# Kernel tuning notes

Measured on AMD Instinct MI355X. Metric: run time of the kernel, lower is better.

Reference implementation:

```python
import jax, jax.numpy as jnp
import numpy as np

N = 14          # num_nodes (fixed by train_adj_14 / BatchNorm1d(14))
BN_EPS = 1e-5
COS_EPS = 1e-8  # torch.cosine_similarity norm clamp


def _leaky(y):
    return jnp.where(y >= 0, y, 0.2 * y)


def _gcn(x, adj, w, b):
    # DenseGCNConv with add_loop=True. adj: [N,N] or [B,N,N]; x: [B,N,F]
    eye = jnp.eye(N, dtype=adj.dtype)
    adj = adj * (1.0 - eye) + eye                    # set diagonal to 1
    d = jnp.clip(adj.sum(-1), 1.0, None) ** -0.5     # [.., N]
    adj = d[..., :, None] * adj * d[..., None, :]    # sym-normalized
    return jnp.matmul(adj, jnp.matmul(x, w)) + b


def _bn(y, gamma, beta):
    # BatchNorm1d(num_features=N) on [B, N, C], training-mode batch stats
    mu = y.mean(axis=(0, 2), keepdims=True)
    var = ((y - mu) ** 2).mean(axis=(0, 2), keepdims=True)
    yhat = (y - mu) * jax.lax.rsqrt(var + BN_EPS)
    return yhat * gamma[None, :, None] + beta[None, :, None]


def _corr(h):
    # vectorized abs cosine-similarity matrix, diag forced to 1
    sq = jnp.sum(h * h, axis=-1, keepdims=True)
    hn = h * jax.lax.rsqrt(jnp.maximum(sq, COS_EPS * COS_EPS))
    c = jnp.abs(jnp.einsum('bif,bjf->bij', hn, hn))
    eye = jnp.eye(N, dtype=c.dtype)
    return c * (1.0 - eye) + eye


def setup_inputs() -> dict:
    key = jax.random.key(0)
    ks = jax.random.split(key, 8)
    B, F_IN, F_OUT = 4096, 1024, 1024
    H = F_OUT // 2

    def sym(k):
        a = jax.random.uniform(k, (N, N), jnp.float32)
        return (a + a.T) * 0.5

    s_fc = (2.0 / (F_IN + F_OUT)) ** 0.5
    s1 = (6.0 / (F_IN + H)) ** 0.5
    s2 = (6.0 / (H + F_OUT)) ** 0.5
    return {
        'x': jax.random.normal(ks[0], (B, N, F_IN), jnp.float32),
        'adj1': sym(ks[1]),
        'adj2': sym(ks[2]),
        'fc_w': jax.random.normal(ks[3], (F_IN, F_OUT), jnp.float32) * s_fc,
        'fc_b': jnp.zeros((F_OUT,), jnp.float32),
        'gcn1_w': jax.random.uniform(ks[4], (F_IN, H), jnp.float32, -s1, s1),
        'gcn1_b': jnp.zeros((H,), jnp.float32),
        'gcn2_w': jax.random.uniform(ks[5], (H, F_OUT), jnp.float32, -s2, s2),
        'gcn2_b': jnp.zeros((F_OUT,), jnp.float32),
        'gamma1': jnp.ones((N,), jnp.float32), 'beta1': jnp.zeros((N,), jnp.float32),
        'gamma2': jnp.ones((N,), jnp.float32), 'beta2': jnp.zeros((N,), jnp.float32),
        'gamma3': jnp.ones((N,), jnp.float32), 'beta3': jnp.zeros((N,), jnp.float32),
    }


def reference(x, adj1, adj2, fc_w, fc_b, gcn1_w, gcn1_b, gcn2_w, gcn2_b,
              gamma1, beta1, gamma2, beta2, gamma3, beta3):
    h = _leaky(jnp.matmul(x, fc_w) + fc_b)           # fc + LeakyReLU(0.2)
    corr = _corr(h)                                   # [B,N,N]

    out = _leaky(_bn(_gcn(x, adj1, gcn1_w, gcn1_b), gamma1, beta1))
    out3 = _leaky(_bn(_gcn(x, adj2, gcn1_w, gcn1_b), gamma3, beta3))
    out4 = _leaky(_bn(_gcn(out3, corr, gcn2_w, gcn2_b), gamma2, beta2))
    out2 = _leaky(_bn(_gcn(out, corr, gcn2_w, gcn2_b), gamma2, beta2))

    return (out2 + out4, corr, h)
```

## Files before the change

### kernel.cpp

```cpp
#include <hip/hip_runtime.h>
#include <stdint.h>

typedef __attribute__((ext_vector_type(8))) short short8;
typedef __attribute__((ext_vector_type(4))) float floatx4;

#define B_SZ 4096
#define M1 57344
#define M2 114688
#define NCAT 1536

#define OFF_XB    ((size_t)0)
#define OFF_BCAT  ((size_t)117440512)
#define OFF_W2T   ((size_t)120586240)
#define OFF_T     ((size_t)121634816)
#define OFF_ADJN  ((size_t)356515840)
#define OFF_ADJC  ((size_t)356517888)
#define OFF_PART1 ((size_t)359729152)
#define OFF_PART2 ((size_t)360646656)
#define OFF_SS1   ((size_t)361564160)
#define OFF_SS2   ((size_t)361564416)

__device__ __forceinline__ unsigned short f2bf(float f){
  union { float f; uint32_t u; } v; v.f = f;
  uint32_t r = (v.u + 0x7FFFu + ((v.u >> 16) & 1u)) >> 16;
  return (unsigned short)r;
}
__device__ __forceinline__ float bf2f(unsigned short s){
  union { uint32_t u; float f; } v; v.u = ((uint32_t)s) << 16; return v.f;
}
__device__ __forceinline__ float leaky(float y){ return y >= 0.0f ? y : 0.2f*y; }
__device__ __forceinline__ void gl2lds16(const void* g, void* l){
  __builtin_amdgcn_global_load_lds(
      (const __attribute__((address_space(1))) unsigned int*)g,
      (__attribute__((address_space(3))) unsigned int*)l, 16, 0, 0);
}

__global__ void k_prep_adj(const float* __restrict__ adj1, const float* __restrict__ adj2,
                           float* __restrict__ adjn){
  __shared__ float a[392];
  __shared__ float d[28];
  int tid = threadIdx.x;
  for (int e = tid; e < 392; e += 256){
    int t = e / 196, ij = e % 196, i = ij / 14, j = ij % 14;
    const float* src = t ? adj2 : adj1;
    a[e] = (i == j) ? 1.0f : src[ij];
  }
  __syncthreads();
  if (tid < 28){
    int t = tid / 14, i = tid % 14;
    float s = 0.f;
    for (int j = 0; j < 14; j++) s += a[t*196 + i*14 + j];
    d[tid] = rsqrtf(fmaxf(s, 1.0f));
  }
  __syncthreads();
  for (int e = tid; e < 392; e += 256){
    int t = e / 196, ij = e % 196, i = ij / 14, j = ij % 14;
    adjn[e] = d[t*14+i] * a[e] * d[t*14+j];
  }
}

__global__ void k_convert_x(const float4* __restrict__ x4, uint2* __restrict__ xb4, int n4){
  int stride = gridDim.x * blockDim.x;
  for (int i = blockIdx.x*blockDim.x + threadIdx.x; i < n4; i += stride){
    float4 f = x4[i];
    uint2 o;
    o.x = (uint32_t)f2bf(f.x) | ((uint32_t)f2bf(f.y) << 16);
    o.y = (uint32_t)f2bf(f.z) | ((uint32_t)f2bf(f.w) << 16);
    xb4[i] = o;
  }
}

__global__ void k_convert_w(const float* __restrict__ fcw, const float* __restrict__ w1,
                            const float* __restrict__ w2, unsigned short* __restrict__ bcatT,
                            unsigned short* __restrict__ w2T){
  int idx = blockIdx.x*blockDim.x + threadIdx.x;
  if (idx < NCAT*1024){
    int n = idx >> 10, k = idx & 1023;
    float v = (n < 1024) ? fcw[k*1024 + n] : w1[k*512 + (n - 1024)];
    bcatT[idx] = f2bf(v);
  } else {
    int r = idx - NCAT*1024;
    int n = r >> 9, k = r & 511;
    w2T[r] = f2bf(w2[k*1024 + n]);
  }
}

template<int MODE>
__global__ __launch_bounds__(256)
void k_gemm_bt(const unsigned short* __restrict__ A, const unsigned short* __restrict__ Bt,
               int K, const float* __restrict__ bias,
               float* __restrict__ h_out, unsigned short* __restrict__ o_bf16){
  __shared__ unsigned short As[4096];
  __shared__ unsigned short Bs[4096];
  int tid = threadIdx.x;
  int lane = tid & 63, wave = tid >> 6;
  int wm = wave & 1, wn = wave >> 1;
  int bm = blockIdx.x, bn = blockIdx.y;
  const unsigned short* aptr = A  + (size_t)(bm*128 + (tid >> 2))*K + (tid & 3)*8;
  const unsigned short* bptr = Bt + (size_t)(bn*128 + (tid >> 2))*K + (tid & 3)*8;
  unsigned short* asd = &As[tid*8];
  unsigned short* bsd = &Bs[tid*8];
  size_t row64 = (size_t)64 * K;
  int fr = lane & 15, fq = lane >> 4;
  floatx4 acc[4][4] = {};
  for (int k0 = 0; k0 < K; k0 += 32){
    __syncthreads();
    gl2lds16(aptr + k0,         asd);
    gl2lds16(aptr + k0 + row64, asd + 2048);
    gl2lds16(bptr + k0,         bsd);
    gl2lds16(bptr + k0 + row64, bsd + 2048);
    __syncthreads();
    short8 af[4], bq[4];
    #pragma unroll
    for (int i = 0; i < 4; i++)
      af[i] = *(const short8*)&As[(wm*64 + i*16 + fr)*32 + fq*8];
    #pragma unroll
    for (int j = 0; j < 4; j++)
      bq[j] = *(const short8*)&Bs[(wn*64 + j*16 + fr)*32 + fq*8];
    #pragma unroll
    for (int i = 0; i < 4; i++)
      #pragma unroll
      for (int j = 0; j < 4; j++)
        acc[i][j] = __builtin_amdgcn_mfma_f32_16x16x32_bf16(af[i], bq[j], acc[i][j], 0, 0, 0);
  }
  #pragma unroll
  for (int i = 0; i < 4; i++){
    #pragma unroll
    for (int j = 0; j < 4; j++){
      int n  = bn*128 + wn*64 + j*16 + fr;
      int mb = bm*128 + wm*64 + i*16 + fq*4;
      #pragma unroll
      for (int r = 0; r < 4; r++){
        int m = mb + r;
        float c = acc[i][j][r];
        if (MODE == 1){
          if (n < 1024){
            c += bias[n];
            h_out[(size_t)m*1024 + n] = leaky(c);
          } else {
            o_bf16[(size_t)m*512 + (n - 1024)] = f2bf(c);
          }
        } else {
          o_bf16[(size_t)m*1024 + n] = f2bf(c);
        }
      }
    }
  }
}

__global__ __launch_bounds__(256)
void k_corr(const float* __restrict__ h, float* __restrict__ corr, float* __restrict__ adjc){
  __shared__ float G[4][16][17];
  __shared__ float C[4][14][15];
  __shared__ float dd[4][16];
  int lane = threadIdx.x & 63, wave = threadIdx.x >> 6;
  int b = blockIdx.x*4 + wave;
  int r = lane & 15, q = lane >> 4;
  const float* hrow = h + (size_t)(b*14 + r)*1024 + q*8;
  bool valid = r < 14;
  floatx4 acc = {0.f, 0.f, 0.f, 0.f};
  for (int k0 = 0; k0 < 1024; k0 += 32){
    short8 f = {0,0,0,0,0,0,0,0};
    if (valid){
      float4 f0 = *(const float4*)(hrow + k0);
      float4 f1 = *(const float4*)(hrow + k0 + 4);
      f[0] = (short)f2bf(f0.x); f[1] = (short)f2bf(f0.y);
      f[2] = (short)f2bf(f0.z); f[3] = (short)f2bf(f0.w);
      f[4] = (short)f2bf(f1.x); f[5] = (short)f2bf(f1.y);
      f[6] = (short)f2bf(f1.z); f[7] = (short)f2bf(f1.w);
    }
    acc = __builtin_amdgcn_mfma_f32_16x16x32_bf16(f, f, acc, 0, 0, 0);
  }
  #pragma unroll
  for (int t = 0; t < 4; t++) G[wave][q*4 + t][r] = acc[t];
  __syncthreads();
  if (lane < 14) dd[wave][lane] = rsqrtf(fmaxf(G[wave][lane][lane], 1e-16f));
  __syncthreads();
  for (int e = lane; e < 196; e += 64){
    int i = e / 14, j = e % 14;
    float c = (i == j) ? 1.0f : fabsf(G[wave][i][j]) * dd[wave][i] * dd[wave][j];
    C[wave][i][j] = c;
    corr[(size_t)b*196 + e] = c;
  }
  __syncthreads();
  if (lane < 14){
    float s = 0.f;
    #pragma unroll
    for (int j = 0; j < 14; j++) s += C[wave][lane][j];
    dd[wave][lane] = rsqrtf(fmaxf(s, 1.0f));
  }
  __syncthreads();
  for (int e = lane; e < 196; e += 64){
    int i = e / 14, j = e % 14;
    adjc[(size_t)b*196 + e] = C[wave][i][j] * dd[wave][i] * dd[wave][j];
  }
}

__global__ __launch_bounds__(256)
void k_stats1(const unsigned short* __restrict__ t1, const float* __restrict__ adjn,
              const float* __restrict__ b1, float* __restrict__ part){
  __shared__ float adjs[392];
  __shared__ float red[56*4];
  int tid = threadIdx.x, b = blockIdx.x;
  for (int e = tid; e < 392; e += 256) adjs[e] = adjn[e];
  __syncthreads();
  int cc = tid*2;
  const unsigned short* base = t1 + (size_t)b*14*512 + cc;
  float v0[14], v1[14];
  #pragma unroll
  for (int m = 0; m < 14; m++){
    unsigned int u = *(const unsigned int*)(base + m*512);
    v0[m] = bf2f((unsigned short)(u & 0xffffu));
    v1[m] = bf2f((unsigned short)(u >> 16));
  }
  float bias0 = b1[cc], bias1 = b1[cc+1];
  float vals[56];
  #pragma unroll
  for (int br = 0; br < 2; br++){
    #pragma unroll
    for (int n = 0; n < 14; n++){
      float p0 = bias0, p1 = bias1;
      const float* arow = &adjs[br*196 + n*14];
      #pragma unroll
      for (int m = 0; m < 14; m++){ p0 += arow[m]*v0[m]; p1 += arow[m]*v1[m]; }
      vals[(br*14 + n)*2 + 0] = p0 + p1;
      vals[(br*14 + n)*2 + 1] = p0*p0 + p1*p1;
    }
  }
  int lane = tid & 63, wave = tid >> 6;
  #pragma unroll
  for (int i = 0; i < 56; i++){
    float x = vals[i];
    #pragma unroll
    for (int off = 32; off > 0; off >>= 1) x += __shfl_down(x, off, 64);
    if (lane == 0) red[i*4 + wave] = x;
  }
  __syncthreads();
  if (tid < 56)
    part[(size_t)tid*4096 + b] = red[tid*4] + red[tid*4+1] + red[tid*4+2] + red[tid*4+3];
}

__global__ void k_finalize(const float* __restrict__ part, const float* __restrict__ gA,
                           const float* __restrict__ bA, const float* __restrict__ gB,
                           const float* __restrict__ bB, float inv_count,
                           float* __restrict__ ss){
  int j = blockIdx.x, tid = threadIdx.x;
  const float* ps = part + (size_t)(j*2)*4096;
  const float* pq = ps + 4096;
  float s = 0.f, q = 0.f;
  for (int e = tid; e < 4096; e += 256){ s += ps[e]; q += pq[e]; }
  __shared__ float rs[4], rq[4];
  int lane = tid & 63, wave = tid >> 6;
  #pragma unroll
  for (int off = 32; off > 0; off >>= 1){ s += __shfl_down(s,off,64); q += __shfl_down(q,off,64); }
  if (lane == 0){ rs[wave] = s; rq[wave] = q; }
  __syncthreads();
  if (tid == 0){
    s = rs[0]+rs[1]+rs[2]+rs[3];
    q = rq[0]+rq[1]+rq[2]+rq[3];
    float mu = s * inv_count;
    float var = q * inv_count - mu*mu;
    float rsig = rsqrtf(var + 1e-5f);
    int br = j / 14, n = j % 14;
    float g  = br ? gB[n] : gA[n];
    float be = br ? bB[n] : bA[n];
    float scale = rsig * g;
    ss[j*2]   = scale;
    ss[j*2+1] = be - mu*scale;
  }
}

__global__ __launch_bounds__(256)
void k_apply1(const unsigned short* __restrict__ t1, const float* __restrict__ adjn,
              const float* __restrict__ b1, const float* __restrict__ ss,
              unsigned short* __restrict__ outcat){
  __shared__ float adjs[392];
  __shared__ float sss[56];
  int tid = threadIdx.x, b = blockIdx.x;
  for (int e = tid; e < 392; e += 256) adjs[e] = adjn[e];
  if (tid < 56) sss[tid] = ss[tid];
  __syncthreads();
  int cc = tid*2;
  const unsigned short* base = t1 + (size_t)b*14*512 + cc;
  float v0[14], v1[14];
  #pragma unroll
  for (int m = 0; m < 14; m++){
    unsigned int u = *(const unsigned int*)(base + m*512);
    v0[m] = bf2f((unsigned short)(u & 0xffffu));
    v1[m] = bf2f((unsigned short)(u >> 16));
  }
  float bias0 = b1[cc], bias1 = b1[cc+1];
  #pragma unroll
  for (int br = 0; br < 2; br++){
    #pragma unroll
    for (int n = 0; n < 14; n++){
      float p0 = bias0, p1 = bias1;
      const float* arow = &adjs[br*196 + n*14];
      #pragma unroll
      for (int m = 0; m < 14; m++){ p0 += arow[m]*v0[m]; p1 += arow[m]*v1[m]; }
      float scale = sss[(br*14+n)*2], shift = sss[(br*14+n)*2+1];
      float y0 = leaky(p0*scale + shift);
      float y1 = leaky(p1*scale + shift);
      size_t row = (size_t)br*M1 + (size_t)b*14 + n;
      *(unsigned int*)(outcat + row*512 + cc) =
          (uint32_t)f2bf(y0) | ((uint32_t)f2bf(y1) << 16);
    }
  }
}

__global__ __launch_bounds__(512)
void k_stats2(const unsigned short* __restrict__ t2, const float* __restrict__ adjc,
              const float* __restrict__ b2, float* __restrict__ part){
  __shared__ float adjs[196];
  __shared__ float red[28*8];
  int tid = threadIdx.x, b = blockIdx.x;
  for (int e = tid; e < 196; e += 512) adjs[e] = adjc[(size_t)b*196 + e];
  __syncthreads();
  int cc = tid*2;
  float bias0 = b2[cc], bias1 = b2[cc+1];
  int lane = tid & 63, wave = tid >> 6;
  for (int half = 0; half < 2; half++){
    const unsigned short* base = t2 + ((size_t)half*M1 + (size_t)b*14)*1024 + cc;
    float v0[14], v1[14];
    #pragma unroll
    for (int m = 0; m < 14; m++){
      unsigned int u = *(const unsigned int*)(base + (size_t)m*1024);
      v0[m] = bf2f((unsigned short)(u & 0xffffu));
      v1[m] = bf2f((unsigned short)(u >> 16));
    }
    float vals[28];
    #pragma unroll
    for (int n = 0; n < 14; n++){
      float p0 = bias0, p1 = bias1;
      const float* arow = &adjs[n*14];
      #pragma unroll
      for (int m = 0; m < 14; m++){ p0 += arow[m]*v0[m]; p1 += arow[m]*v1[m]; }
      vals[n*2]   = p0 + p1;
      vals[n*2+1] = p0*p0 + p1*p1;
    }
    #pragma unroll
    for (int i = 0; i < 28; i++){
      float x = vals[i];
      #pragma unroll
      for (int off = 32; off > 0; off >>= 1) x += __shfl_down(x, off, 64);
      if (lane == 0) red[i*8 + wave] = x;
    }
    __syncthreads();
    if (tid < 28){
      float x = 0.f;
      #pragma unroll
      for (int w = 0; w < 8; w++) x += red[tid*8 + w];
      part[(size_t)(half*28 + tid)*4096 + b] = x;
    }
    __syncthreads();
  }
}

__global__ __launch_bounds__(512)
void k_apply2(const unsigned short* __restrict__ t2, const float* __restrict__ adjc,
              const float* __restrict__ b2, const float* __restrict__ ss,
              float* __restrict__ out){
  __shared__ float adjs[196];
  __shared__ float sss[56];
  int tid = threadIdx.x, b = blockIdx.x;
  for (int e = tid; e < 196; e += 512) adjs[e] = adjc[(size_t)b*196 + e];
  if (tid < 56) sss[tid] = ss[tid];
  __syncthreads();
  int cc = tid*2;
  float bias0 = b2[cc], bias1 = b2[cc+1];
  const unsigned short* base2 = t2 + ((size_t)b*14)*1024 + cc;
  const unsigned short* base4 = t2 + ((size_t)M1 + (size_t)b*14)*1024 + cc;
  float v20[14], v21[14], v40[14], v41[14];
  #pragma unroll
  for (int m = 0; m < 14; m++){
    unsigned int u = *(const unsigned int*)(base2 + (size_t)m*1024);
    v20[m] = bf2f((unsigned short)(u & 0xffffu)); v21[m] = bf2f((unsigned short)(u >> 16));
    unsigned int w = *(const unsigned int*)(base4 + (size_t)m*1024);
    v40[m] = bf2f((unsigned short)(w & 0xffffu)); v41[m] = bf2f((unsigned short)(w >> 16));
  }
  #pragma unroll
  for (int n = 0; n < 14; n++){
    float p20 = bias0, p21 = bias1, p40 = bias0, p41 = bias1;
    const float* arow = &adjs[n*14];
    #pragma unroll
    for (int m = 0; m < 14; m++){
      float a = arow[m];
      p20 += a*v20[m]; p21 += a*v21[m]; p40 += a*v40[m]; p41 += a*v41[m];
    }
    float s2 = sss[n*2],      h2 = sss[n*2+1];
    float s4 = sss[28 + n*2], h4 = sss[28 + n*2+1];
    float2 o;
    o.x = leaky(p20*s2 + h2) + leaky(p40*s4 + h4);
    o.y = leaky(p21*s2 + h2) + leaky(p41*s4 + h4);
    *(float2*)(out + ((size_t)b*14 + n)*1024 + cc) = o;
  }
}

extern "C" void kernel_launch(void* const* d_in, const int* in_sizes, int n_in,
                              void* d_out, int out_size, void* d_ws, size_t ws_size,
                              hipStream_t stream){
  const float* x      = (const float*)d_in[0];
  const float* adj1   = (const float*)d_in[1];
  const float* adj2   = (const float*)d_in[2];
  const float* fc_w   = (const float*)d_in[3];
  const float* fc_b   = (const float*)d_in[4];
  const float* g1w    = (const float*)d_in[5];
  const float* g1b    = (const float*)d_in[6];
  const float* g2w    = (const float*)d_in[7];
  const float* g2b    = (const float*)d_in[8];
  const float* gamma1 = (const float*)d_in[9];
  const float* beta1  = (const float*)d_in[10];
  const float* gamma2 = (const float*)d_in[11];
  const float* beta2  = (const float*)d_in[12];
  const float* gamma3 = (const float*)d_in[13];
  const float* beta3  = (const float*)d_in[14];

  float* out_main = (float*)d_out;
  float* out_corr = out_main + (size_t)M1*1024;
  float* out_h    = out_corr + (size_t)B_SZ*196;

  char* ws = (char*)d_ws;
  unsigned short* xb     = (unsigned short*)(ws + OFF_XB);
  unsigned short* outcat = (unsigned short*)(ws + OFF_XB);
  unsigned short* bcatT  = (unsigned short*)(ws + OFF_BCAT);
  unsigned short* w2T    = (unsigned short*)(ws + OFF_W2T);
  unsigned short* t1     = (unsigned short*)(ws + OFF_T);
  unsigned short* t2     = (unsigned short*)(ws + OFF_T);
  float* adjn  = (float*)(ws + OFF_ADJN);
  float* adjc  = (float*)(ws + OFF_ADJC);
  float* part1 = (float*)(ws + OFF_PART1);
  float* part2 = (float*)(ws + OFF_PART2);
  float* ss1   = (float*)(ws + OFF_SS1);
  float* ss2   = (float*)(ws + OFF_SS2);

  k_prep_adj<<<1, 256, 0, stream>>>(adj1, adj2, adjn);
  k_convert_x<<<8192, 256, 0, stream>>>((const float4*)x, (uint2*)xb, 14680064);
  k_convert_w<<<8192, 256, 0, stream>>>(fc_w, g1w, g2w, bcatT, w2T);
  k_gemm_bt<1><<<dim3(448, 12), 256, 0, stream>>>(xb, bcatT, 1024, fc_b, out_h, t1);
  k_corr<<<1024, 256, 0, stream>>>(out_h, out_corr, adjc);
  k_stats1<<<4096, 256, 0, stream>>>(t1, adjn, g1b, part1);
  k_finalize<<<28, 256, 0, stream>>>(part1, gamma1, beta1, gamma3, beta3,
                                     1.0f/(4096.0f*512.0f), ss1);
  k_apply1<<<4096, 256, 0, stream>>>(t1, adjn, g1b, ss1, outcat);
  k_gemm_bt<2><<<dim3(896, 8), 256, 0, stream>>>(outcat, w2T, 512, nullptr, nullptr, t2);
  k_stats2<<<4096, 512, 0, stream>>>(t2, adjc, g2b, part2);
  k_finalize<<<28, 256, 0, stream>>>(part2, gamma2, beta2, gamma2, beta2,
                                     1.0f/(4096.0f*1024.0f), ss2);
  k_apply2<<<4096, 512, 0, stream>>>(t2, adjc, g2b, ss2, out_main);
}
```

Baseline: 1.870 ms.

## Tile weight transpose through LDS, remap GEMM blocks per XCD, split corr K

```diff
diff --git a/kernel.cpp b/kernel.cpp
--- a/kernel.cpp
+++ b/kernel.cpp
@@ -70,22 +70,41 @@
   }
 }
 
-__global__ void k_convert_w(const float* __restrict__ fcw, const float* __restrict__ w1,
-                            const float* __restrict__ w2, unsigned short* __restrict__ bcatT,
-                            unsigned short* __restrict__ w2T){
-  int idx = blockIdx.x*blockDim.x + threadIdx.x;
-  if (idx < NCAT*1024){
-    int n = idx >> 10, k = idx & 1023;
-    float v = (n < 1024) ? fcw[k*1024 + n] : w1[k*512 + (n - 1024)];
-    bcatT[idx] = f2bf(v);
+__global__ __launch_bounds__(256)
+void k_convert_w(const float* __restrict__ fcw, const float* __restrict__ w1,
+                 const float* __restrict__ w2, unsigned short* __restrict__ bcatT,
+                 unsigned short* __restrict__ w2T){
+  __shared__ float tile[64][65];
+  int id = blockIdx.x, tid = threadIdx.x;
+  const float* src; unsigned short* dst;
+  int lds_src, ldo, row_off, tk, tn;
+  if (id < 256){
+    src = fcw; dst = bcatT; lds_src = 1024; ldo = 1024; row_off = 0;
+    tk = id & 15; tn = id >> 4;
+  } else if (id < 384){
+    int r = id - 256;
+    src = w1; dst = bcatT; lds_src = 512; ldo = 1024; row_off = 1024;
+    tk = r & 15; tn = r >> 4;
   } else {
-    int r = idx - NCAT*1024;
-    int n = r >> 9, k = r & 511;
-    w2T[r] = f2bf(w2[k*1024 + n]);
-  }
-}
-
-template<int MODE>
+    int r = id - 384;
+    src = w2; dst = w2T; lds_src = 1024; ldo = 512; row_off = 0;
+    tk = r & 7; tn = r >> 3;
+  }
+  int c = tid & 63, r0 = tid >> 6;
+  #pragma unroll
+  for (int i = 0; i < 16; i++){
+    int kr = r0 + i*4;
+    tile[kr][c] = src[(size_t)(tk*64 + kr)*lds_src + tn*64 + c];
+  }
+  __syncthreads();
+  #pragma unroll
+  for (int i = 0; i < 16; i++){
+    int nr = r0 + i*4;
+    dst[(size_t)(row_off + tn*64 + nr)*ldo + tk*64 + c] = f2bf(tile[c][nr]);
+  }
+}
+
+template<int MODE, int NT>
 __global__ __launch_bounds__(256)
 void k_gemm_bt(const unsigned short* __restrict__ A, const unsigned short* __restrict__ Bt,
                int K, const float* __restrict__ bias,
@@ -95,7 +114,11 @@
   int tid = threadIdx.x;
   int lane = tid & 63, wave = tid >> 6;
   int wm = wave & 1, wn = wave >> 1;
-  int bm = blockIdx.x, bn = blockIdx.y;
+  int cpx = gridDim.x >> 3;
+  int orig = blockIdx.x;
+  int wgid = (orig & 7) * cpx + (orig >> 3);
+  int bn = wgid % NT;
+  int bm = wgid / NT;
   const unsigned short* aptr = A  + (size_t)(bm*128 + (tid >> 2))*K + (tid & 3)*8;
   const unsigned short* bptr = Bt + (size_t)(bn*128 + (tid >> 2))*K + (tid & 3)*8;
   unsigned short* asd = &As[tid*8];
@@ -150,16 +173,19 @@
 
 __global__ __launch_bounds__(256)
 void k_corr(const float* __restrict__ h, float* __restrict__ corr, float* __restrict__ adjc){
-  __shared__ float G[4][16][17];
-  __shared__ float C[4][14][15];
-  __shared__ float dd[4][16];
-  int lane = threadIdx.x & 63, wave = threadIdx.x >> 6;
-  int b = blockIdx.x*4 + wave;
+  __shared__ float G[2][16][17];
+  __shared__ float Gh[2][16][17];
+  __shared__ float C[2][14][15];
+  __shared__ float dd[2][16];
+  int tid = threadIdx.x;
+  int lane = tid & 63, wave = tid >> 6;
+  int s = wave >> 1, kh = wave & 1;
+  int b = blockIdx.x*2 + s;
   int r = lane & 15, q = lane >> 4;
-  const float* hrow = h + (size_t)(b*14 + r)*1024 + q*8;
+  const float* hrow = h + (size_t)(b*14 + r)*1024 + kh*512 + q*8;
   bool valid = r < 14;
   floatx4 acc = {0.f, 0.f, 0.f, 0.f};
-  for (int k0 = 0; k0 < 1024; k0 += 32){
+  for (int k0 = 0; k0 < 512; k0 += 32){
     short8 f = {0,0,0,0,0,0,0,0};
     if (valid){
       float4 f0 = *(const float4*)(hrow + k0);
@@ -171,28 +197,38 @@
     }
     acc = __builtin_amdgcn_mfma_f32_16x16x32_bf16(f, f, acc, 0, 0, 0);
   }
-  #pragma unroll
-  for (int t = 0; t < 4; t++) G[wave][q*4 + t][r] = acc[t];
-  __syncthreads();
-  if (lane < 14) dd[wave][lane] = rsqrtf(fmaxf(G[wave][lane][lane], 1e-16f));
-  __syncthreads();
-  for (int e = lane; e < 196; e += 64){
-    int i = e / 14, j = e % 14;
-    float c = (i == j) ? 1.0f : fabsf(G[wave][i][j]) * dd[wave][i] * dd[wave][j];
-    C[wave][i][j] = c;
-    corr[(size_t)b*196 + e] = c;
-  }
-  __syncthreads();
-  if (lane < 14){
-    float s = 0.f;
-    #pragma unroll
-    for (int j = 0; j < 14; j++) s += C[wave][lane][j];
-    dd[wave][lane] = rsqrtf(fmaxf(s, 1.0f));
-  }
-  __syncthreads();
-  for (int e = lane; e < 196; e += 64){
-    int i = e / 14, j = e % 14;
-    adjc[(size_t)b*196 + e] = C[wave][i][j] * dd[wave][i] * dd[wave][j];
+  float* gdst = kh ? &Gh[s][0][0] : &G[s][0][0];
+  #pragma unroll
+  for (int t = 0; t < 4; t++) gdst[(q*4 + t)*17 + r] = acc[t];
+  __syncthreads();
+  for (int e = tid; e < 512; e += 256){
+    int ss = e >> 8, ij = e & 255, i = ij >> 4, j = ij & 15;
+    G[ss][i][j] += Gh[ss][i][j];
+  }
+  __syncthreads();
+  if (tid < 28){
+    int ss = tid / 14, i = tid % 14;
+    dd[ss][i] = rsqrtf(fmaxf(G[ss][i][i], 1e-16f));
+  }
+  __syncthreads();
+  for (int e = tid; e < 392; e += 256){
+    int ss = e / 196, ij = e % 196, i = ij / 14, j = ij % 14;
+    float c = (i == j) ? 1.0f : fabsf(G[ss][i][j]) * dd[ss][i] * dd[ss][j];
+    C[ss][i][j] = c;
+    corr[(size_t)(blockIdx.x*2 + ss)*196 + ij] = c;
+  }
+  __syncthreads();
+  if (tid < 28){
+    int ss = tid / 14, i = tid % 14;
+    float sum = 0.f;
+    #pragma unroll
+    for (int j = 0; j < 14; j++) sum += C[ss][i][j];
+    dd[ss][i] = rsqrtf(fmaxf(sum, 1.0f));
+  }
+  __syncthreads();
+  for (int e = tid; e < 392; e += 256){
+    int ss = e / 196, ij = e % 196, i = ij / 14, j = ij % 14;
+    adjc[(size_t)(blockIdx.x*2 + ss)*196 + ij] = C[ss][i][j] * dd[ss][i] * dd[ss][j];
   }
 }
 
@@ -435,14 +471,14 @@
 
   k_prep_adj<<<1, 256, 0, stream>>>(adj1, adj2, adjn);
   k_convert_x<<<8192, 256, 0, stream>>>((const float4*)x, (uint2*)xb, 14680064);
-  k_convert_w<<<8192, 256, 0, stream>>>(fc_w, g1w, g2w, bcatT, w2T);
-  k_gemm_bt<1><<<dim3(448, 12), 256, 0, stream>>>(xb, bcatT, 1024, fc_b, out_h, t1);
-  k_corr<<<1024, 256, 0, stream>>>(out_h, out_corr, adjc);
+  k_convert_w<<<512, 256, 0, stream>>>(fc_w, g1w, g2w, bcatT, w2T);
+  k_gemm_bt<1, 12><<<5376, 256, 0, stream>>>(xb, bcatT, 1024, fc_b, out_h, t1);
+  k_corr<<<2048, 256, 0, stream>>>(out_h, out_corr, adjc);
   k_stats1<<<4096, 256, 0, stream>>>(t1, adjn, g1b, part1);
   k_finalize<<<28, 256, 0, stream>>>(part1, gamma1, beta1, gamma3, beta3,
                                      1.0f/(4096.0f*512.0f), ss1);
   k_apply1<<<4096, 256, 0, stream>>>(t1, adjn, g1b, ss1, outcat);
-  k_gemm_bt<2><<<dim3(896, 8), 256, 0, stream>>>(outcat, w2T, 512, nullptr, nullptr, t2);
+  k_gemm_bt<2, 8><<<7168, 256, 0, stream>>>(outcat, w2T, 512, nullptr, nullptr, t2);
   k_stats2<<<4096, 512, 0, stream>>>(t2, adjc, g2b, part2);
   k_finalize<<<28, 256, 0, stream>>>(part2, gamma2, beta2, gamma2, beta2,
                                      1.0f/(4096.0f*1024.0f), ss2);
```

Result: faster. 1.812 ms (-3.1%).
